# Optimization experiments

Hardware: AMD Instinct MI355X
Metric: run time of the kernel (lower is better)

The kernel has to match this reference:

```python
import jax, jax.numpy as jnp
import numpy as np

N = 8192
IN_F = 512
OUT_F = 128


def setup_inputs() -> dict:
    key = jax.random.key(0)
    k1, k2, k3, k4, k5, k6 = jax.random.split(key, 6)
    inp = jax.random.normal(k1, (N, IN_F), dtype=jnp.float32)
    adj = jax.random.randint(k2, (N, N), 0, 2).astype(jnp.float32)
    M = jax.random.uniform(k3, (N, N), dtype=jnp.float32)
    W = jax.random.normal(k4, (IN_F, OUT_F), dtype=jnp.float32) * (1.414 * np.sqrt(2.0 / (IN_F + OUT_F)))
    a_self = jax.random.normal(k5, (OUT_F, 1), dtype=jnp.float32) * (1.414 * np.sqrt(2.0 / (OUT_F + 1)))
    a_neighs = jax.random.normal(k6, (OUT_F, 1), dtype=jnp.float32) * (1.414 * np.sqrt(2.0 / (OUT_F + 1)))
    return {"input": inp, "adj": adj, "M": M, "W": W, "a_self": a_self, "a_neighs": a_neighs}


def reference(input, adj, M, W, a_self, a_neighs):
    h = input @ W                       # [N, OUT_F]
    attn_self = h @ a_self              # [N, 1]
    attn_neighs = h @ a_neighs          # [N, 1]
    e = attn_self + attn_neighs.T       # [N, N] broadcast add
    e = jax.nn.leaky_relu(e * M, negative_slope=0.2)
    e = jnp.where(adj > 0, e, jnp.float32(-9e15))
    attention = jax.nn.softmax(e, axis=1)
    h_prime = attention @ h             # [N, OUT_F]
    return jax.nn.elu(h_prime)          # concat=True
```

## Files before the change

### kernel.cpp

```cpp
#include <hip/hip_runtime.h>
#include <hip/hip_bf16.h>

typedef __attribute__((ext_vector_type(4))) float f32x4;
typedef __attribute__((ext_vector_type(8))) short s16x8;

constexpr int NN   = 8192;
constexpr int KIN  = 512;
constexpr int KOUT = 128;

constexpr int JCHUNK = 4;
constexpr int JLEN   = NN / JCHUNK;
constexpr int SG     = 32;
constexpr int NS     = JLEN / SG;
constexpr int BUFSTRIDE = 24576;
constexpr int A_OFF = 8192;
constexpr int H_OFF = 16384;
constexpr int T_OFF = 73728;

__device__ __forceinline__ ushort f2bf(float x) {
    union { float f; unsigned u; } v; v.f = x;
    unsigned r = (v.u + 0x7fffu + ((v.u >> 16) & 1u)) >> 16;
    return (ushort)r;
}

__device__ __forceinline__ void gload_lds16(const void* g, void* l) {
    __builtin_amdgcn_global_load_lds((const __attribute__((address_space(1))) void*)g,
                                     (__attribute__((address_space(3))) void*)l, 16, 0, 0);
}

__global__ __launch_bounds__(256) void kA(const float* __restrict__ inp,
                                          const float* __restrict__ W,
                                          const float* __restrict__ a_s,
                                          const float* __restrict__ a_n,
                                          ushort* __restrict__ hT,
                                          float* __restrict__ s_out,
                                          float* __restrict__ t_out) {
    __shared__ float smem[16 * 512];
    const int t = threadIdx.x;
    const int rbase = blockIdx.x * 16;

#pragma unroll
    for (int it = 0; it < 8; ++it) {
        int idx = it * 256 + t;
        int r = idx >> 7;
        int c4 = (idx & 127) << 2;
        *(f32x4*)(&smem[r * 512 + c4]) =
            *(const f32x4*)(inp + (size_t)(rbase + r) * KIN + c4);
    }
    __syncthreads();

    const int c0 = (t & 31) * 4;
    const int rg = (t >> 5) * 2;
    float acc[2][4] = {};
#pragma unroll 4
    for (int k = 0; k < KIN; ++k) {
        f32x4 w4 = *(const f32x4*)(W + (size_t)k * KOUT + c0);
        float a0 = smem[(rg + 0) * 512 + k];
        float a1 = smem[(rg + 1) * 512 + k];
#pragma unroll
        for (int cc = 0; cc < 4; ++cc) {
            acc[0][cc] += a0 * w4[cc];
            acc[1][cc] += a1 * w4[cc];
        }
    }
    __syncthreads();

    float* h_lds = smem;
#pragma unroll
    for (int rr = 0; rr < 2; ++rr) {
        f32x4 v = {acc[rr][0], acc[rr][1], acc[rr][2], acc[rr][3]};
        *(f32x4*)(&h_lds[(rg + rr) * 128 + c0]) = v;
    }
    __syncthreads();

    {
        const int col = t >> 1;
        const int r0 = (t & 1) * 8;
        ushort tmp[8];
#pragma unroll
        for (int rr = 0; rr < 8; ++rr) tmp[rr] = f2bf(h_lds[(r0 + rr) * 128 + col]);
        *(f32x4*)(hT + (size_t)col * NN + rbase + r0) = *(f32x4*)&tmp[0];
    }

    {
        const int w = t >> 6, lane = t & 63;
        float as1 = a_s[lane], as2 = a_s[64 + lane];
        float an1 = a_n[lane], an2 = a_n[64 + lane];
#pragma unroll
        for (int rr = 0; rr < 4; ++rr) {
            int row = w * 4 + rr;
            float h1 = h_lds[row * 128 + lane];
            float h2 = h_lds[row * 128 + 64 + lane];
            float ps = h1 * as1 + h2 * as2;
            float pt = h1 * an1 + h2 * an2;
#pragma unroll
            for (int off = 32; off; off >>= 1) {
                ps += __shfl_xor(ps, off);
                pt += __shfl_xor(pt, off);
            }
            if (lane == 0) {
                s_out[rbase + row] = ps;
                t_out[rbase + row] = pt;
            }
        }
    }
}

__global__ __launch_bounds__(256, 2) void kB(const float* __restrict__ Mmat,
                                             const float* __restrict__ adjm,
                                             const ushort* __restrict__ hT,
                                             const float* __restrict__ s_in,
                                             const float* __restrict__ t_in,
                                             float* __restrict__ o_part,
                                             float* __restrict__ l_part) {
    __shared__ f32x4 LDSQ[81920 / 16];
    char* LDS = (char*)LDSQ;

    const int tid = threadIdx.x;
    const int w = tid >> 6;
    const int l = tid & 63;
    const int lrow = l & 15;
    const int kgrp = l >> 4;
    const int rb = blockIdx.x >> 2;
    const int jc = blockIdx.x & 3;
    const int j0 = jc * JLEN;

    {
        const float* tp = t_in + j0 + tid * 8;
        f32x4 a = *(const f32x4*)tp;
        f32x4 b = *(const f32x4*)(tp + 4);
        *(f32x4*)(LDS + T_OFF + tid * 32) = a;
        *(f32x4*)(LDS + T_OFF + tid * 32 + 16) = b;
    }
    asm volatile("s_waitcnt lgkmcnt(0)" ::: "memory");

    const float si = s_in[rb * 64 + w * 16 + lrow];

    const int rl8 = l >> 3, c8 = l & 7;
    const int csMA = c8 ^ rl8;
    const float* gM0 = Mmat + (size_t)(rb * 64 + w * 16 + rl8) * NN + j0 + csMA * 4;
    const float* gM1 = gM0 + (size_t)8 * NN;
    const float* gA0 = adjm + (size_t)(rb * 64 + w * 16 + rl8) * NN + j0 + csMA * 4;
    const float* gA1 = gA0 + (size_t)8 * NN;
    const int rl4 = l >> 2, c4 = l & 3;
    const int csH = c4 ^ (rl8 & 3);
    const ushort* gH0 = hT + (size_t)(w * 32 + rl4) * NN + j0 + csH * 8;
    const ushort* gH1 = gH0 + (size_t)16 * NN;

    const int mdst0 = (w * 16) * 128, mdst1 = (w * 16 + 8) * 128;
    const int hdst0 = (w * 32) * 64, hdst1 = (w * 32 + 16) * 64;

    const int Cm0 = (w * 16 + lrow) * 128 + (((kgrp * 2 + 0) ^ (lrow & 7)) << 4);
    const int Cm1 = (w * 16 + lrow) * 128 + (((kgrp * 2 + 1) ^ (lrow & 7)) << 4);
    const int Ch  = lrow * 64 + ((kgrp ^ ((lrow >> 1) & 3)) << 4);

    f32x4 acc[8];
#pragma unroll
    for (int ct = 0; ct < 8; ++ct) acc[ct] = (f32x4){0.f, 0.f, 0.f, 0.f};
    float lsum = 0.f;

#define ISSUE(BB)                                                  \
    gload_lds16(gM0, LDS + (BB) + mdst0);                          \
    gload_lds16(gM1, LDS + (BB) + mdst1);                          \
    gload_lds16(gA0, LDS + (BB) + A_OFF + mdst0);                  \
    gload_lds16(gA1, LDS + (BB) + A_OFF + mdst1);                  \
    gload_lds16(gH0, LDS + (BB) + H_OFF + hdst0);                  \
    gload_lds16(gH1, LDS + (BB) + H_OFF + hdst1);

#define ADV()                                                      \
    gM0 += SG; gM1 += SG; gA0 += SG; gA1 += SG; gH0 += SG; gH1 += SG;

    ISSUE(0)
    ADV()
    ISSUE(BUFSTRIDE)
    ADV()

    unsigned b0 = 0, b1 = BUFSTRIDE, b2 = 2 * BUFSTRIDE;

#pragma unroll 1
    for (int s = 0; s < NS; ++s) {
        asm volatile("s_waitcnt vmcnt(6)" ::: "memory");
        __builtin_amdgcn_s_barrier();
        asm volatile("" ::: "memory");

        ISSUE(b2)
        if (s + 3 < NS) { ADV() }

        {
            const char* tb = LDS + T_OFF + s * 128 + kgrp * 32;
            f32x4 tv0 = *(const f32x4*)tb;
            f32x4 tv1 = *(const f32x4*)(tb + 16);
            f32x4 mv0 = *(const f32x4*)(LDS + b0 + Cm0);
            f32x4 mv1 = *(const f32x4*)(LDS + b0 + Cm1);
            f32x4 av0 = *(const f32x4*)(LDS + b0 + A_OFF + Cm0);
            f32x4 av1 = *(const f32x4*)(LDS + b0 + A_OFF + Cm1);

            s16x8 af;
#pragma unroll
            for (int e = 0; e < 4; ++e) {
                float x = (si + tv0[e]) * mv0[e];
                x = fmaxf(x, 0.2f * x);
                float p = __expf(x) * av0[e];
                lsum += p;
                af[e] = (short)f2bf(p);
            }
#pragma unroll
            for (int e = 0; e < 4; ++e) {
                float x = (si + tv1[e]) * mv1[e];
                x = fmaxf(x, 0.2f * x);
                float p = __expf(x) * av1[e];
                lsum += p;
                af[4 + e] = (short)f2bf(p);
            }

            const char* hb = LDS + b0 + H_OFF + Ch;
#pragma unroll
            for (int ct = 0; ct < 8; ++ct) {
                s16x8 bf = *(const s16x8*)(hb + ct * 1024);
                acc[ct] = __builtin_amdgcn_mfma_f32_16x16x32_bf16(af, bf, acc[ct], 0, 0, 0);
            }
        }

        unsigned bt = b0; b0 = b1; b1 = b2; b2 = bt;
    }
#undef ISSUE
#undef ADV

    lsum += __shfl_xor(lsum, 16);
    lsum += __shfl_xor(lsum, 32);
    if (l < 16) l_part[(size_t)jc * NN + rb * 64 + w * 16 + lrow] = lsum;

    float* op = o_part + (size_t)jc * NN * KOUT;
#pragma unroll
    for (int ct = 0; ct < 8; ++ct) {
#pragma unroll
        for (int r = 0; r < 4; ++r) {
            int gi = rb * 64 + w * 16 + kgrp * 4 + r;
            int col = ct * 16 + lrow;
            op[(size_t)gi * KOUT + col] = acc[ct][r];
        }
    }
}

__global__ __launch_bounds__(256) void kC(const float* __restrict__ o_part,
                                          const float* __restrict__ l_part,
                                          float* __restrict__ out) {
    const int idx = blockIdx.x * 256 + threadIdx.x;
    const int i = idx >> 7;
    float osum = 0.f, lsum = 0.f;
#pragma unroll
    for (int p = 0; p < JCHUNK; ++p) {
        osum += o_part[(size_t)p * NN * KOUT + idx];
        lsum += l_part[(size_t)p * NN + i];
    }
    float v = osum / lsum;
    out[idx] = v > 0.f ? v : (__expf(v) - 1.f);
}

extern "C" void kernel_launch(void* const* d_in, const int* in_sizes, int n_in,
                              void* d_out, int out_size, void* d_ws, size_t ws_size,
                              hipStream_t stream) {
    const float* inp = (const float*)d_in[0];
    const float* adj = (const float*)d_in[1];
    const float* Mm  = (const float*)d_in[2];
    const float* W   = (const float*)d_in[3];
    const float* a_s = (const float*)d_in[4];
    const float* a_n = (const float*)d_in[5];
    float* out = (float*)d_out;

    char* ws = (char*)d_ws;
    ushort* hT    = (ushort*)(ws + 0);
    float*  s_buf = (float*)(ws + 2097152);
    float*  t_buf = (float*)(ws + 2129920);
    float*  l_prt = (float*)(ws + 2162688);
    float*  o_prt = (float*)(ws + 4194304);

    hipLaunchKernelGGL(kA, dim3(512), dim3(256), 0, stream, inp, W, a_s, a_n, hT, s_buf, t_buf);
    hipLaunchKernelGGL(kB, dim3(128 * JCHUNK), dim3(256), 0, stream, Mm, adj, hT, s_buf, t_buf, o_prt, l_prt);
    hipLaunchKernelGGL(kC, dim3(4096), dim3(256), 0, stream, o_prt, l_prt, out);
}
```

Baseline: 211.2 us.

## Pack adjacency into bitmask, drop T staging, atomically accumulate outputs

A new prep kernel compresses the float adjacency matrix into a 1-bit-per-entry mask. The main attention kernel then streams only M and h through LDS, selecting masked entries with bit tests. Dropping the adjacency tile shrinks the LDS footprint, which allows 3 blocks per CU and splitting the column range into 8 chunks. The t vector is now register-prefetched instead of staged in LDS, and partial outputs are combined with atomicAdd into a zeroed buffer rather than summed from per-chunk arrays in the final kernel. The cost is an extra full pass over adj in the prep kernel, a memset, and atomic contention plus nondeterministic summation order.

```diff
diff --git a/kernel.cpp b/kernel.cpp
--- a/kernel.cpp
+++ b/kernel.cpp
@@ -8,14 +8,12 @@
 constexpr int KIN  = 512;
 constexpr int KOUT = 128;
 
-constexpr int JCHUNK = 4;
+constexpr int JCHUNK = 8;
 constexpr int JLEN   = NN / JCHUNK;
 constexpr int SG     = 32;
 constexpr int NS     = JLEN / SG;
-constexpr int BUFSTRIDE = 24576;
-constexpr int A_OFF = 8192;
-constexpr int H_OFF = 16384;
-constexpr int T_OFF = 73728;
+constexpr int BUFSTRIDE = 16384;
+constexpr int H_OFF = 8192;
 
 __device__ __forceinline__ ushort f2bf(float x) {
     union { float f; unsigned u; } v; v.f = x;
@@ -26,6 +24,20 @@
 __device__ __forceinline__ void gload_lds16(const void* g, void* l) {
     __builtin_amdgcn_global_load_lds((const __attribute__((address_space(1))) void*)g,
                                      (__attribute__((address_space(3))) void*)l, 16, 0, 0);
+}
+
+__global__ __launch_bounds__(256) void kPrep(const float* __restrict__ adjm,
+                                             unsigned* __restrict__ bm) {
+    const int wi = blockIdx.x * 256 + threadIdx.x;
+    const float* p = adjm + (size_t)wi * 32;
+    unsigned b = 0;
+#pragma unroll
+    for (int q = 0; q < 8; ++q) {
+        f32x4 v = *(const f32x4*)(p + q * 4);
+#pragma unroll
+        for (int e = 0; e < 4; ++e) b |= (v[e] > 0.f ? 1u : 0u) << (q * 4 + e);
+    }
+    bm[wi] = b;
 }
 
 __global__ __launch_bounds__(256) void kA(const float* __restrict__ inp,
@@ -106,14 +118,14 @@
     }
 }
 
-__global__ __launch_bounds__(256, 2) void kB(const float* __restrict__ Mmat,
-                                             const float* __restrict__ adjm,
+__global__ __launch_bounds__(256, 3) void kB(const float* __restrict__ Mmat,
+                                             const unsigned* __restrict__ bm,
                                              const ushort* __restrict__ hT,
                                              const float* __restrict__ s_in,
                                              const float* __restrict__ t_in,
-                                             float* __restrict__ o_part,
+                                             float* __restrict__ o_acc,
                                              float* __restrict__ l_part) {
-    __shared__ f32x4 LDSQ[81920 / 16];
+    __shared__ f32x4 LDSQ[49152 / 16];
     char* LDS = (char*)LDSQ;
 
     const int tid = threadIdx.x;
@@ -121,38 +133,31 @@
     const int l = tid & 63;
     const int lrow = l & 15;
     const int kgrp = l >> 4;
-    const int rb = blockIdx.x >> 2;
-    const int jc = blockIdx.x & 3;
+    const int rb = blockIdx.x >> 3;
+    const int jc = blockIdx.x & 7;
     const int j0 = jc * JLEN;
-
-    {
-        const float* tp = t_in + j0 + tid * 8;
-        f32x4 a = *(const f32x4*)tp;
-        f32x4 b = *(const f32x4*)(tp + 4);
-        *(f32x4*)(LDS + T_OFF + tid * 32) = a;
-        *(f32x4*)(LDS + T_OFF + tid * 32 + 16) = b;
-    }
-    asm volatile("s_waitcnt lgkmcnt(0)" ::: "memory");
-
-    const float si = s_in[rb * 64 + w * 16 + lrow];
+    const int i = rb * 64 + w * 16 + lrow;
+
+    const float si = s_in[i];
 
     const int rl8 = l >> 3, c8 = l & 7;
     const int csMA = c8 ^ rl8;
     const float* gM0 = Mmat + (size_t)(rb * 64 + w * 16 + rl8) * NN + j0 + csMA * 4;
     const float* gM1 = gM0 + (size_t)8 * NN;
-    const float* gA0 = adjm + (size_t)(rb * 64 + w * 16 + rl8) * NN + j0 + csMA * 4;
-    const float* gA1 = gA0 + (size_t)8 * NN;
     const int rl4 = l >> 2, c4 = l & 3;
     const int csH = c4 ^ (rl8 & 3);
     const ushort* gH0 = hT + (size_t)(w * 32 + rl4) * NN + j0 + csH * 8;
     const ushort* gH1 = gH0 + (size_t)16 * NN;
 
     const int mdst0 = (w * 16) * 128, mdst1 = (w * 16 + 8) * 128;
-    const int hdst0 = (w * 32) * 64, hdst1 = (w * 32 + 16) * 64;
+    const int hdst0 = H_OFF + (w * 32) * 64, hdst1 = H_OFF + (w * 32 + 16) * 64;
 
     const int Cm0 = (w * 16 + lrow) * 128 + (((kgrp * 2 + 0) ^ (lrow & 7)) << 4);
     const int Cm1 = (w * 16 + lrow) * 128 + (((kgrp * 2 + 1) ^ (lrow & 7)) << 4);
-    const int Ch  = lrow * 64 + ((kgrp ^ ((lrow >> 1) & 3)) << 4);
+    const int Ch  = H_OFF + lrow * 64 + ((kgrp ^ ((lrow >> 1) & 3)) << 4);
+
+    const unsigned* bwp = bm + (size_t)i * 256 + (j0 >> 5);
+    const float* tp = t_in + j0 + kgrp * 8;
 
     f32x4 acc[8];
 #pragma unroll
@@ -162,16 +167,16 @@
 #define ISSUE(BB)                                                  \
     gload_lds16(gM0, LDS + (BB) + mdst0);                          \
     gload_lds16(gM1, LDS + (BB) + mdst1);                          \
-    gload_lds16(gA0, LDS + (BB) + A_OFF + mdst0);                  \
-    gload_lds16(gA1, LDS + (BB) + A_OFF + mdst1);                  \
-    gload_lds16(gH0, LDS + (BB) + H_OFF + hdst0);                  \
-    gload_lds16(gH1, LDS + (BB) + H_OFF + hdst1);
-
-#define ADV()                                                      \
-    gM0 += SG; gM1 += SG; gA0 += SG; gA1 += SG; gH0 += SG; gH1 += SG;
+    gload_lds16(gH0, LDS + (BB) + hdst0);                          \
+    gload_lds16(gH1, LDS + (BB) + hdst1);
+
+#define ADV() gM0 += SG; gM1 += SG; gH0 += SG; gH1 += SG;
 
     ISSUE(0)
     ADV()
+    unsigned mk = bwp[0];
+    f32x4 ta0 = *(const f32x4*)(tp);
+    f32x4 ta1 = *(const f32x4*)(tp + 4);
     ISSUE(BUFSTRIDE)
     ADV()
 
@@ -179,41 +184,43 @@
 
 #pragma unroll 1
     for (int s = 0; s < NS; ++s) {
-        asm volatile("s_waitcnt vmcnt(6)" ::: "memory");
+        asm volatile("s_waitcnt vmcnt(4)" ::: "memory");
         __builtin_amdgcn_s_barrier();
         asm volatile("" ::: "memory");
 
+        const int sn = (s + 1 < NS) ? (s + 1) : s;
+        unsigned mk_n = bwp[sn];
+        f32x4 tn0 = *(const f32x4*)(tp + sn * SG);
+        f32x4 tn1 = *(const f32x4*)(tp + sn * SG + 4);
+
         ISSUE(b2)
         if (s + 3 < NS) { ADV() }
 
         {
-            const char* tb = LDS + T_OFF + s * 128 + kgrp * 32;
-            f32x4 tv0 = *(const f32x4*)tb;
-            f32x4 tv1 = *(const f32x4*)(tb + 16);
             f32x4 mv0 = *(const f32x4*)(LDS + b0 + Cm0);
             f32x4 mv1 = *(const f32x4*)(LDS + b0 + Cm1);
-            f32x4 av0 = *(const f32x4*)(LDS + b0 + A_OFF + Cm0);
-            f32x4 av1 = *(const f32x4*)(LDS + b0 + A_OFF + Cm1);
 
             s16x8 af;
 #pragma unroll
             for (int e = 0; e < 4; ++e) {
-                float x = (si + tv0[e]) * mv0[e];
+                float x = (si + ta0[e]) * mv0[e];
                 x = fmaxf(x, 0.2f * x);
-                float p = __expf(x) * av0[e];
+                float p = __expf(x);
+                p = ((mk >> (kgrp * 8 + e)) & 1u) ? p : 0.f;
                 lsum += p;
                 af[e] = (short)f2bf(p);
             }
 #pragma unroll
             for (int e = 0; e < 4; ++e) {
-                float x = (si + tv1[e]) * mv1[e];
+                float x = (si + ta1[e]) * mv1[e];
                 x = fmaxf(x, 0.2f * x);
-                float p = __expf(x) * av1[e];
+                float p = __expf(x);
+                p = ((mk >> (kgrp * 8 + 4 + e)) & 1u) ? p : 0.f;
                 lsum += p;
                 af[4 + e] = (short)f2bf(p);
             }
 
-            const char* hb = LDS + b0 + H_OFF + Ch;
+            const char* hb = LDS + b0 + Ch;
 #pragma unroll
             for (int ct = 0; ct < 8; ++ct) {
                 s16x8 bf = *(const s16x8*)(hb + ct * 1024);
@@ -221,6 +228,7 @@
             }
         }
 
+        mk = mk_n; ta0 = tn0; ta1 = tn1;
         unsigned bt = b0; b0 = b1; b1 = b2; b2 = bt;
     }
 #undef ISSUE
@@ -228,32 +236,28 @@
 
     lsum += __shfl_xor(lsum, 16);
     lsum += __shfl_xor(lsum, 32);
-    if (l < 16) l_part[(size_t)jc * NN + rb * 64 + w * 16 + lrow] = lsum;
-
-    float* op = o_part + (size_t)jc * NN * KOUT;
+    if (l < 16) l_part[(size_t)jc * NN + i] = lsum;
+
 #pragma unroll
     for (int ct = 0; ct < 8; ++ct) {
 #pragma unroll
         for (int r = 0; r < 4; ++r) {
             int gi = rb * 64 + w * 16 + kgrp * 4 + r;
             int col = ct * 16 + lrow;
-            op[(size_t)gi * KOUT + col] = acc[ct][r];
-        }
-    }
-}
-
-__global__ __launch_bounds__(256) void kC(const float* __restrict__ o_part,
+            atomicAdd(&o_acc[(size_t)gi * KOUT + col], acc[ct][r]);
+        }
+    }
+}
+
+__global__ __launch_bounds__(256) void kC(const float* __restrict__ o_acc,
                                           const float* __restrict__ l_part,
                                           float* __restrict__ out) {
     const int idx = blockIdx.x * 256 + threadIdx.x;
     const int i = idx >> 7;
-    float osum = 0.f, lsum = 0.f;
-#pragma unroll
-    for (int p = 0; p < JCHUNK; ++p) {
-        osum += o_part[(size_t)p * NN * KOUT + idx];
-        lsum += l_part[(size_t)p * NN + i];
-    }
-    float v = osum / lsum;
+    float lsum = 0.f;
+#pragma unroll
+    for (int p = 0; p < JCHUNK; ++p) lsum += l_part[(size_t)p * NN + i];
+    float v = o_acc[idx] / lsum;
     out[idx] = v > 0.f ? v : (__expf(v) - 1.f);
 }
 
@@ -269,13 +273,16 @@
     float* out = (float*)d_out;
 
     char* ws = (char*)d_ws;
-    ushort* hT    = (ushort*)(ws + 0);
-    float*  s_buf = (float*)(ws + 2097152);
-    float*  t_buf = (float*)(ws + 2129920);
-    float*  l_prt = (float*)(ws + 2162688);
-    float*  o_prt = (float*)(ws + 4194304);
-
+    ushort*   hT    = (ushort*)(ws + 0);
+    float*    s_buf = (float*)(ws + 2097152);
+    float*    t_buf = (float*)(ws + 2129920);
+    float*    l_prt = (float*)(ws + 2162688);
+    float*    o_acc = (float*)(ws + 4194304);
+    unsigned* bmask = (unsigned*)(ws + 8388608);
+
+    hipMemsetAsync(o_acc, 0, (size_t)NN * KOUT * sizeof(float), stream);
+    hipLaunchKernelGGL(kPrep, dim3(NN * NN / 32 / 256), dim3(256), 0, stream, adj, bmask);
     hipLaunchKernelGGL(kA, dim3(512), dim3(256), 0, stream, inp, W, a_s, a_n, hT, s_buf, t_buf);
-    hipLaunchKernelGGL(kB, dim3(128 * JCHUNK), dim3(256), 0, stream, Mm, adj, hT, s_buf, t_buf, o_prt, l_prt);
-    hipLaunchKernelGGL(kC, dim3(4096), dim3(256), 0, stream, o_prt, l_prt, out);
-}
+    hipLaunchKernelGGL(kB, dim3(128 * JCHUNK), dim3(256), 0, stream, Mm, bmask, hT, s_buf, t_buf, o_acc, l_prt);
+    hipLaunchKernelGGL(kC, dim3(4096), dim3(256), 0, stream, o_acc, l_prt, out);
+}
```

Result: slower. 242.9 us (+15.0%).
